# Performance work log

Measured on AMD Instinct MI355X. Metric: run time of the kernel, lower is better.

The kernel has to match this reference:

```python
import jax, jax.numpy as jnp
import numpy as np

B, T, C, H = 8, 2048, 384, 64

def setup_inputs() -> dict:
    key = jax.random.key(0)
    k1, k2, k3, k4 = jax.random.split(key, 4)
    x = jax.random.normal(k1, (B, T, C), dtype=jnp.float32)
    Wq = jax.random.normal(k2, (C, H), dtype=jnp.float32) * (C ** -0.5)
    Wk = jax.random.normal(k3, (C, H), dtype=jnp.float32) * (C ** -0.5)
    Wv = jax.random.normal(k4, (C, H), dtype=jnp.float32) * (C ** -0.5)
    return {"x": x, "Wq": Wq, "Wk": Wk, "Wv": Wv}

def reference(x, Wq, Wk, Wv):
    # x: (B, T, C); projections: (B, T, H)
    Bn, Tn, Cn = x.shape
    q = jnp.einsum('btc,ch->bth', x, Wq)
    k = jnp.einsum('btc,ch->bth', x, Wk)
    v = jnp.einsum('btc,ch->bth', x, Wv)
    # NOTE: source scales by C**-0.5 (embedding dim), not head_size**-0.5
    weights = jnp.einsum('bth,bsh->bts', q, k) * (Cn ** -0.5)  # (B, T, T)
    causal = jnp.tril(jnp.ones((Tn, Tn), dtype=bool))
    weights = jnp.where(causal, weights, -jnp.inf)
    # NOTE: source applies softmax over dim=1 (query/row axis), reproduced faithfully
    weights = jax.nn.softmax(weights, axis=1)
    # dropout omitted (eval-mode reference)
    return jnp.einsum('bts,bsh->bth', weights, v)
```

## Files before the change

### kernel.cpp

```cpp
#include <hip/hip_runtime.h>
#include <hip/hip_bf16.h>
#include <math.h>

#define Bn 8
#define Tn 2048
#define Cn 384
#define Hn 64
#define SCALE2 0.07362241f

using bf16x8 = __attribute__((ext_vector_type(8))) short;
using f32x4  = __attribute__((ext_vector_type(4))) float;
using u32x4  = __attribute__((ext_vector_type(4))) unsigned;

#define MFMA(a, b, c) __builtin_amdgcn_mfma_f32_16x16x32_bf16((a), (b), (c), 0, 0, 0)

static __device__ __forceinline__ short f2bf(float f) {
  unsigned u = __float_as_uint(f);
  u += 0x7fffu + ((u >> 16) & 1u);
  return (short)(u >> 16);
}
static __device__ __forceinline__ float bf2f(short s) {
  return __uint_as_float(((unsigned)(unsigned short)s) << 16);
}
static __device__ __forceinline__ float fexp2(float x) {
#if __has_builtin(__builtin_amdgcn_exp2f)
  return __builtin_amdgcn_exp2f(x);
#else
  return exp2f(x);
#endif
}
static __device__ __forceinline__ unsigned pack2(float lo, float hi) {
  return (unsigned)(unsigned short)f2bf(lo) | ((unsigned)(unsigned short)f2bf(hi) << 16);
}

__global__ __launch_bounds__(256) void wconv_kernel(
    const float* __restrict__ Wq, const float* __restrict__ Wk,
    const float* __restrict__ Wv, short* __restrict__ WbT) {
  int idx = blockIdx.x * 256 + threadIdx.x;
  int n = idx / 384, k = idx - n * 384;
  const float* W = (n < 64) ? Wq : (n < 128) ? Wk : Wv;
  WbT[idx] = f2bf(W[k * 64 + (n & 63)]);
}

__global__ __launch_bounds__(256) void proj_kernel(
    const float* __restrict__ x, const short* __restrict__ WbT,
    short* __restrict__ qb, short* __restrict__ kb, short* __restrict__ vT) {
  __shared__ short xs[16][392];
  __shared__ short vtile[64][20];
  const int tid = threadIdx.x;
  const int t0 = blockIdx.x * 16;
  const float* xb = x + (size_t)t0 * Cn;
  #pragma unroll
  for (int i = 0; i < 6; ++i) {
    int j = tid + i * 256;
    int row = j / 96, colv = (j - row * 96) * 4;
    float4 v = *(const float4*)(xb + row * Cn + colv);
    short4 s4; s4.x = f2bf(v.x); s4.y = f2bf(v.y); s4.z = f2bf(v.z); s4.w = f2bf(v.w);
    *(short4*)(&xs[row][colv]) = s4;
  }
  __syncthreads();
  const int w = tid >> 6, l15 = tid & 15, quad = (tid & 63) >> 4;
  f32x4 acc[3] = {};
  for (int ks = 0; ks < 12; ++ks) {
    bf16x8 a = *(const bf16x8*)(&xs[l15][ks * 32 + quad * 8]);
    #pragma unroll
    for (int cf = 0; cf < 3; ++cf) {
      bf16x8 bfr = *(const bf16x8*)(WbT + (size_t)(48 * w + 16 * cf + l15) * Cn + ks * 32 + quad * 8);
      acc[cf] = MFMA(a, bfr, acc[cf]);
    }
  }
  #pragma unroll
  for (int cf = 0; cf < 3; ++cf) {
    int cbase = 48 * w + 16 * cf, c = cbase + l15;
    #pragma unroll
    for (int r = 0; r < 4; ++r) {
      int row = t0 + quad * 4 + r;
      short val = f2bf(acc[cf][r]);
      if (cbase < 64)       qb[(size_t)row * Hn + c] = val;
      else if (cbase < 128) kb[(size_t)row * Hn + (c - 64)] = val;
      else                  vtile[c - 128][quad * 4 + r] = val;
    }
  }
  __syncthreads();
  const int b = t0 >> 11, t0l = t0 & 2047;
  int h = tid >> 2, tseg = (tid & 3) * 4;
  *(short4*)(vT + ((size_t)(b * Hn + h)) * Tn + t0l + tseg) =
      *(const short4*)(&vtile[h][tseg]);
}

__global__ __launch_bounds__(256) void colstats_kernel(
    const short* __restrict__ qb, const short* __restrict__ kb,
    float* __restrict__ pL) {
  const int unit = blockIdx.x;
  const int b = unit >> 7, rem = unit & 127;
  const int j = rem >> 3, u = rem & 7;
  const int lo = (u * 33) >> 3, hi = ((u + 1) * 33) >> 3;
  const int big = 32 - j;
  const int tid = threadIdx.x, w = tid >> 6, l15 = tid & 15, quad = (tid & 63) >> 4;
  __shared__ float redl[64][17];

  auto run = [&](const int i, const int k0, const int k1, const int slot) {
    const int s0 = i << 6;
    float l[4] = {0.f, 0.f, 0.f, 0.f};
    const int n = k1 - k0;
    if (n > 0) {
      bf16x8 bk[8];
      #pragma unroll
      for (int nf = 0; nf < 4; ++nf) {
        const size_t krow = (size_t)(b * Tn + s0 + 16 * nf + l15) * Hn;
        bk[2 * nf]     = *(const bf16x8*)(kb + krow + quad * 8);
        bk[2 * nf + 1] = *(const bf16x8*)(kb + krow + 32 + quad * 8);
      }
      auto cload = [&](bf16x8& A0, bf16x8& A1, int k) {
        size_t ar = (size_t)(b * Tn + ((i + k) << 6) + 16 * w + l15) * Hn;
        A0 = *(const bf16x8*)(qb + ar + quad * 8);
        A1 = *(const bf16x8*)(qb + ar + 32 + quad * 8);
      };
      auto ccomp = [&](bf16x8 A0, bf16x8 A1, int k) {
        f32x4 sc[4] = {};
        #pragma unroll
        for (int nf = 0; nf < 4; ++nf) {
          sc[nf] = MFMA(A0, bk[2 * nf], sc[nf]);
          sc[nf] = MFMA(A1, bk[2 * nf + 1], sc[nf]);
        }
        const bool diag = (k == 0);
        const int tb = ((i + k) << 6) + 16 * w + quad * 4;
        #pragma unroll
        for (int nf = 0; nf < 4; ++nf) {
          int s = s0 + 16 * nf + l15;
          #pragma unroll
          for (int r = 0; r < 4; ++r) {
            float v = sc[nf][r] * SCALE2;
            if (diag && (tb + r) < s) v = -INFINITY;
            l[nf] += fexp2(v);
          }
        }
      };
      bf16x8 a0A, a1A, a0B, a1B, a0C, a1C;
      cload(a0A, a1A, k0);
      if (n > 1) cload(a0B, a1B, k0 + 1);
      if (n > 2) cload(a0C, a1C, k0 + 2);
      int k = k0;
      while (k + 3 < k1) {
        ccomp(a0A, a1A, k);     cload(a0A, a1A, k + 3);
        ccomp(a0B, a1B, k + 1); if (k + 4 < k1) cload(a0B, a1B, k + 4);
        ccomp(a0C, a1C, k + 2); if (k + 5 < k1) cload(a0C, a1C, k + 5);
        k += 3;
      }
      const int rem2 = k1 - k;
      if (rem2 > 0) ccomp(a0A, a1A, k);
      if (rem2 > 1) ccomp(a0B, a1B, k + 1);
      if (rem2 > 2) ccomp(a0C, a1C, k + 2);
    }
    __syncthreads();
    #pragma unroll
    for (int nf = 0; nf < 4; ++nf) redl[16 * nf + l15][w * 4 + quad] = l[nf];
    __syncthreads();
    if (tid < 64) {
      float ls = 0.f;
      #pragma unroll
      for (int q2 = 0; q2 < 16; ++q2) ls += redl[tid][q2];
      pL[unit * 128 + slot * 64 + tid] = ls;
    }
  };
  run(j, lo, min(hi, big), 0);
  run(31 - j, max(lo, big) - big, hi - big, 1);
}

__global__ __launch_bounds__(256) void vhat_kernel(
    const short* __restrict__ vT, const float* __restrict__ pL,
    short* __restrict__ vS, float* __restrict__ outz) {
  int gid = blockIdx.x * 256 + threadIdx.x;
  size_t base = (size_t)gid * 8;
  int b = (int)(base >> 17), s = (int)(base & 2047);
  int i = s >> 6, c = s & 63;
  int j2 = (i < 16) ? i : 31 - i;
  int slot = (i < 16) ? 0 : 1;
  const float* pp = pL + (size_t)((b * 16 + j2) * 8) * 128 + slot * 64 + c;
  float L0x = 0.f, L0y = 0.f, L0z = 0.f, L0w = 0.f;
  float L1x = 0.f, L1y = 0.f, L1z = 0.f, L1w = 0.f;
  #pragma unroll
  for (int u = 0; u < 8; ++u) {
    float4 p0 = *(const float4*)(pp + u * 128);
    float4 p1 = *(const float4*)(pp + u * 128 + 4);
    L0x += p0.x; L0y += p0.y; L0z += p0.z; L0w += p0.w;
    L1x += p1.x; L1y += p1.y; L1z += p1.z; L1w += p1.w;
  }
  short4 v0 = *(const short4*)(vT + base);
  short4 v1 = *(const short4*)(vT + base + 4);
  short4 r0, r1;
  r0.x = f2bf(bf2f(v0.x) / L0x); r0.y = f2bf(bf2f(v0.y) / L0y);
  r0.z = f2bf(bf2f(v0.z) / L0z); r0.w = f2bf(bf2f(v0.w) / L0w);
  r1.x = f2bf(bf2f(v1.x) / L1x); r1.y = f2bf(bf2f(v1.y) / L1y);
  r1.z = f2bf(bf2f(v1.z) / L1z); r1.w = f2bf(bf2f(v1.w) / L1w);
  *(short4*)(vS + base) = r0;
  *(short4*)(vS + base + 4) = r1;
  float4 z = {0.f, 0.f, 0.f, 0.f};
  *(float4*)(outz + base) = z;
  *(float4*)(outz + base + 4) = z;
}

__global__ __launch_bounds__(256) void outg_kernel(
    const short* __restrict__ qb, const short* __restrict__ kb,
    const short* __restrict__ vS, float* __restrict__ out) {
  const int unit = blockIdx.x;
  const int b = unit >> 7, rem = unit & 127;
  const int j = rem >> 3, u = rem & 7;
  const int lo = (u * 33) >> 3, hi = ((u + 1) * 33) >> 3;
  const int big = 32 - j;
  const int tid = threadIdx.x, w = tid >> 6, l15 = tid & 15, quad = (tid & 63) >> 4;
  __shared__ unsigned plds_raw[4][512];
  char* pw = (char*)(&plds_raw[w][0]);
  const int swz = (l15 & 7) << 4;
  int wroff[8];
  #pragma unroll
  for (int nf = 0; nf < 4; ++nf)
    #pragma unroll
    for (int p = 0; p < 2; ++p)
      wroff[2 * nf + p] = l15 * 128 + ((nf * 32 + quad * 8 + p * 4) ^ swz);
  const int rd0 = l15 * 128 + ((quad * 16) ^ swz);
  const int rd1 = l15 * 128 + ((64 + quad * 16) ^ swz);
  const size_t QKbase = (size_t)b * Tn * Hn;
  const size_t Vbase  = (size_t)b * Hn * Tn;

  auto run = [&](const int tile, const int k0, const int k1) {
    if (k0 >= k1) return;
    const int tbase = (tile << 6) + 16 * w;
    const size_t qrow = QKbase + (size_t)(tbase + l15) * Hn;
    const bf16x8 qf0 = *(const bf16x8*)(qb + qrow + quad * 8);
    const bf16x8 qf1 = *(const bf16x8*)(qb + qrow + 32 + quad * 8);
    const int tg = tbase + l15;
    f32x4 acc[4] = {};
    bf16x8 kf[8];
    auto loadK = [&](int ch) {
      const int s0 = ch << 6;
      #pragma unroll
      for (int nf = 0; nf < 4; ++nf) {
        const size_t kr = QKbase + (size_t)(s0 + 16 * nf + l15) * Hn;
        kf[2 * nf]     = *(const bf16x8*)(kb + kr + quad * 8);
        kf[2 * nf + 1] = *(const bf16x8*)(kb + kr + 32 + quad * 8);
      }
    };
    loadK(k0);
    for (int ch = k0; ch < k1; ++ch) {
      const int s0 = ch << 6;
      f32x4 sc[4] = {};
      #pragma unroll
      for (int nf = 0; nf < 4; ++nf) {
        sc[nf] = MFMA(kf[2 * nf], qf0, sc[nf]);
        sc[nf] = MFMA(kf[2 * nf + 1], qf1, sc[nf]);
      }
      if (ch + 1 < k1) loadK(ch + 1);
      bf16x8 vf[8];
      #pragma unroll
      for (int nf = 0; nf < 4; ++nf) {
        const size_t vr = Vbase + (size_t)(16 * nf + l15) * Tn + s0;
        vf[2 * nf]     = *(const bf16x8*)(vS + vr + quad * 8);
        vf[2 * nf + 1] = *(const bf16x8*)(vS + vr + 32 + quad * 8);
      }
      const bool diag = (ch == tile);
      #pragma unroll
      for (int nf = 0; nf < 4; ++nf) {
        float ev[4];
        #pragma unroll
        for (int r = 0; r < 4; ++r) {
          float v = sc[nf][r] * SCALE2;
          const int s = s0 + 16 * nf + quad * 4 + r;
          if (diag && tg < s) v = -INFINITY;
          ev[r] = fexp2(v);
        }
        *(unsigned*)(pw + wroff[2 * nf])     = pack2(ev[0], ev[1]);
        *(unsigned*)(pw + wroff[2 * nf + 1]) = pack2(ev[2], ev[3]);
      }
      __asm__ __volatile__("" ::: "memory");
      const bf16x8 a0 = __builtin_bit_cast(bf16x8, *(const u32x4*)(pw + rd0));
      const bf16x8 a1 = __builtin_bit_cast(bf16x8, *(const u32x4*)(pw + rd1));
      #pragma unroll
      for (int nf = 0; nf < 4; ++nf) {
        acc[nf] = MFMA(a0, vf[2 * nf], acc[nf]);
        acc[nf] = MFMA(a1, vf[2 * nf + 1], acc[nf]);
      }
    }
    #pragma unroll
    for (int nf = 0; nf < 4; ++nf)
      #pragma unroll
      for (int r = 0; r < 4; ++r)
        atomicAdd(&out[QKbase + (size_t)(tbase + quad * 4 + r) * Hn + 16 * nf + l15],
                  acc[nf][r]);
  };
  run(31 - j, lo, min(hi, big));
  run(j, max(lo, big) - big, hi - big);
}

extern "C" void kernel_launch(void* const* d_in, const int* in_sizes, int n_in,
                              void* d_out, int out_size, void* d_ws, size_t ws_size,
                              hipStream_t stream) {
  const float* x  = (const float*)d_in[0];
  const float* Wq = (const float*)d_in[1];
  const float* Wk = (const float*)d_in[2];
  const float* Wv = (const float*)d_in[3];
  char* ws = (char*)d_ws;
  short* qb   = (short*)(ws);
  short* kb   = (short*)(ws + 2097152);
  short* vT   = (short*)(ws + 4194304);
  short* vS   = (short*)(ws + 6291456);
  short* WbT  = (short*)(ws + 8388608);
  float* pL   = (float*)(ws + 8536064);
  float* outp = (float*)d_out;

  hipLaunchKernelGGL(wconv_kernel, dim3(288), dim3(256), 0, stream, Wq, Wk, Wv, WbT);
  hipLaunchKernelGGL(proj_kernel, dim3(Bn * Tn / 16), dim3(256), 0, stream, x, WbT, qb, kb, vT);
  hipLaunchKernelGGL(colstats_kernel, dim3(1024), dim3(256), 0, stream, qb, kb, pL);
  hipLaunchKernelGGL(vhat_kernel, dim3(512), dim3(256), 0, stream, vT, pL, vS, outp);
  hipLaunchKernelGGL(outg_kernel, dim3(1024), dim3(256), 0, stream, qb, kb, vS, outp);
}
```

Measured before the change: 162.5 us.

## Split key chunks across waves per 16-row strip and reduce in LDS, dropping atomics

Reworks the output kernel so each block handles one 16-row query strip of a tile, with its four waves striding over key chunks. Partial accumulators are reduced through shared memory and written with plain stores, replacing global atomicAdds and the zero-fill of the output in vhat_kernel. It also prefetches V one chunk ahead, orders blocks so the largest tiles launch first, and sets a launch-bounds occupancy hint. The cost is duplicated Q/K reads per strip, a new LDS reduction buffer, and wave imbalance on small tiles.

```diff
diff --git a/kernel.cpp b/kernel.cpp
--- a/kernel.cpp
+++ b/kernel.cpp
@@ -169,7 +169,7 @@
 
 __global__ __launch_bounds__(256) void vhat_kernel(
     const short* __restrict__ vT, const float* __restrict__ pL,
-    short* __restrict__ vS, float* __restrict__ outz) {
+    short* __restrict__ vS) {
   int gid = blockIdx.x * 256 + threadIdx.x;
   size_t base = (size_t)gid * 8;
   int b = (int)(base >> 17), s = (int)(base & 2047);
@@ -195,101 +195,113 @@
   r1.z = f2bf(bf2f(v1.z) / L1z); r1.w = f2bf(bf2f(v1.w) / L1w);
   *(short4*)(vS + base) = r0;
   *(short4*)(vS + base + 4) = r1;
-  float4 z = {0.f, 0.f, 0.f, 0.f};
-  *(float4*)(outz + base) = z;
-  *(float4*)(outz + base + 4) = z;
-}
-
-__global__ __launch_bounds__(256) void outg_kernel(
+}
+
+__global__ __launch_bounds__(256, 3) void outg_kernel(
     const short* __restrict__ qb, const short* __restrict__ kb,
     const short* __restrict__ vS, float* __restrict__ out) {
-  const int unit = blockIdx.x;
-  const int b = unit >> 7, rem = unit & 127;
-  const int j = rem >> 3, u = rem & 7;
-  const int lo = (u * 33) >> 3, hi = ((u + 1) * 33) >> 3;
-  const int big = 32 - j;
+  const int bid = blockIdx.x;
+  const int tile = 31 - (bid >> 5);
+  const int sub = bid & 31;
+  const int b = sub >> 2, strip = sub & 3;
+  const int nch = tile + 1;
   const int tid = threadIdx.x, w = tid >> 6, l15 = tid & 15, quad = (tid & 63) >> 4;
-  __shared__ unsigned plds_raw[4][512];
-  char* pw = (char*)(&plds_raw[w][0]);
+  __shared__ unsigned plds[4][512];
+  __shared__ float red[4][16][64];
   const int swz = (l15 & 7) << 4;
   int wroff[8];
   #pragma unroll
   for (int nf = 0; nf < 4; ++nf)
     #pragma unroll
     for (int p = 0; p < 2; ++p)
-      wroff[2 * nf + p] = l15 * 128 + ((nf * 32 + quad * 8 + p * 4) ^ swz);
-  const int rd0 = l15 * 128 + ((quad * 16) ^ swz);
-  const int rd1 = l15 * 128 + ((64 + quad * 16) ^ swz);
+      wroff[2 * nf + p] = (l15 * 128 + ((nf * 32 + quad * 8 + p * 4) ^ swz)) >> 2;
+  const int rd0 = (l15 * 128 + ((quad * 16) ^ swz)) >> 2;
+  const int rd1 = (l15 * 128 + ((64 + quad * 16) ^ swz)) >> 2;
   const size_t QKbase = (size_t)b * Tn * Hn;
   const size_t Vbase  = (size_t)b * Hn * Tn;
-
-  auto run = [&](const int tile, const int k0, const int k1) {
-    if (k0 >= k1) return;
-    const int tbase = (tile << 6) + 16 * w;
-    const size_t qrow = QKbase + (size_t)(tbase + l15) * Hn;
-    const bf16x8 qf0 = *(const bf16x8*)(qb + qrow + quad * 8);
-    const bf16x8 qf1 = *(const bf16x8*)(qb + qrow + 32 + quad * 8);
-    const int tg = tbase + l15;
-    f32x4 acc[4] = {};
-    bf16x8 kf[8];
-    auto loadK = [&](int ch) {
-      const int s0 = ch << 6;
+  const int tbase = (tile << 6) + 16 * strip;
+  const int tg = tbase + l15;
+
+  const size_t qrow = QKbase + (size_t)(tbase + l15) * Hn;
+  const bf16x8 qf0 = *(const bf16x8*)(qb + qrow + quad * 8);
+  const bf16x8 qf1 = *(const bf16x8*)(qb + qrow + 32 + quad * 8);
+
+  f32x4 acc[4] = {};
+  bf16x8 kf[8], vf[8];
+  auto loadK = [&](int ch) {
+    const int s0 = ch << 6;
+    #pragma unroll
+    for (int nf = 0; nf < 4; ++nf) {
+      const size_t kr = QKbase + (size_t)(s0 + 16 * nf + l15) * Hn;
+      kf[2 * nf]     = *(const bf16x8*)(kb + kr + quad * 8);
+      kf[2 * nf + 1] = *(const bf16x8*)(kb + kr + 32 + quad * 8);
+    }
+  };
+  auto loadV = [&](int ch) {
+    const int s0 = ch << 6;
+    #pragma unroll
+    for (int nf = 0; nf < 4; ++nf) {
+      const size_t vr = Vbase + (size_t)(16 * nf + l15) * Tn + s0;
+      vf[2 * nf]     = *(const bf16x8*)(vS + vr + quad * 8);
+      vf[2 * nf + 1] = *(const bf16x8*)(vS + vr + 32 + quad * 8);
+    }
+  };
+
+  if (w < nch) { loadK(w); loadV(w); }
+  for (int ch = w; ch < nch; ch += 4) {
+    const int s0 = ch << 6;
+    f32x4 sc[4] = {};
+    #pragma unroll
+    for (int nf = 0; nf < 4; ++nf) {
+      sc[nf] = MFMA(kf[2 * nf], qf0, sc[nf]);
+      sc[nf] = MFMA(kf[2 * nf + 1], qf1, sc[nf]);
+    }
+    const int nx = ch + 4;
+    if (nx < nch) loadK(nx);
+    const bool diag = (ch == tile);
+    #pragma unroll
+    for (int nf = 0; nf < 4; ++nf) {
+      float ev[4];
       #pragma unroll
-      for (int nf = 0; nf < 4; ++nf) {
-        const size_t kr = QKbase + (size_t)(s0 + 16 * nf + l15) * Hn;
-        kf[2 * nf]     = *(const bf16x8*)(kb + kr + quad * 8);
-        kf[2 * nf + 1] = *(const bf16x8*)(kb + kr + 32 + quad * 8);
+      for (int r = 0; r < 4; ++r) {
+        float v = sc[nf][r] * SCALE2;
+        const int s = s0 + 16 * nf + quad * 4 + r;
+        if (diag && tg < s) v = -INFINITY;
+        ev[r] = fexp2(v);
       }
-    };
-    loadK(k0);
-    for (int ch = k0; ch < k1; ++ch) {
-      const int s0 = ch << 6;
-      f32x4 sc[4] = {};
-      #pragma unroll
-      for (int nf = 0; nf < 4; ++nf) {
-        sc[nf] = MFMA(kf[2 * nf], qf0, sc[nf]);
-        sc[nf] = MFMA(kf[2 * nf + 1], qf1, sc[nf]);
-      }
-      if (ch + 1 < k1) loadK(ch + 1);
-      bf16x8 vf[8];
-      #pragma unroll
-      for (int nf = 0; nf < 4; ++nf) {
-        const size_t vr = Vbase + (size_t)(16 * nf + l15) * Tn + s0;
-        vf[2 * nf]     = *(const bf16x8*)(vS + vr + quad * 8);
-        vf[2 * nf + 1] = *(const bf16x8*)(vS + vr + 32 + quad * 8);
-      }
-      const bool diag = (ch == tile);
-      #pragma unroll
-      for (int nf = 0; nf < 4; ++nf) {
-        float ev[4];
-        #pragma unroll
-        for (int r = 0; r < 4; ++r) {
-          float v = sc[nf][r] * SCALE2;
-          const int s = s0 + 16 * nf + quad * 4 + r;
-          if (diag && tg < s) v = -INFINITY;
-          ev[r] = fexp2(v);
-        }
-        *(unsigned*)(pw + wroff[2 * nf])     = pack2(ev[0], ev[1]);
-        *(unsigned*)(pw + wroff[2 * nf + 1]) = pack2(ev[2], ev[3]);
-      }
-      __asm__ __volatile__("" ::: "memory");
-      const bf16x8 a0 = __builtin_bit_cast(bf16x8, *(const u32x4*)(pw + rd0));
-      const bf16x8 a1 = __builtin_bit_cast(bf16x8, *(const u32x4*)(pw + rd1));
-      #pragma unroll
-      for (int nf = 0; nf < 4; ++nf) {
-        acc[nf] = MFMA(a0, vf[2 * nf], acc[nf]);
-        acc[nf] = MFMA(a1, vf[2 * nf + 1], acc[nf]);
-      }
-    }
-    #pragma unroll
-    for (int nf = 0; nf < 4; ++nf)
-      #pragma unroll
-      for (int r = 0; r < 4; ++r)
-        atomicAdd(&out[QKbase + (size_t)(tbase + quad * 4 + r) * Hn + 16 * nf + l15],
-                  acc[nf][r]);
-  };
-  run(31 - j, lo, min(hi, big));
-  run(j, max(lo, big) - big, hi - big);
+      plds[w][wroff[2 * nf]]     = pack2(ev[0], ev[1]);
+      plds[w][wroff[2 * nf + 1]] = pack2(ev[2], ev[3]);
+    }
+    __asm__ __volatile__("" ::: "memory");
+    const bf16x8 a0 = __builtin_bit_cast(bf16x8, *(const u32x4*)(&plds[w][rd0]));
+    const bf16x8 a1 = __builtin_bit_cast(bf16x8, *(const u32x4*)(&plds[w][rd1]));
+    #pragma unroll
+    for (int nf = 0; nf < 4; ++nf) {
+      acc[nf] = MFMA(a0, vf[2 * nf], acc[nf]);
+      acc[nf] = MFMA(a1, vf[2 * nf + 1], acc[nf]);
+    }
+    if (nx < nch) loadV(nx);
+  }
+
+  #pragma unroll
+  for (int nf = 0; nf < 4; ++nf)
+    #pragma unroll
+    for (int r = 0; r < 4; ++r)
+      red[w][quad * 4 + r][16 * nf + l15] = acc[nf][r];
+  __syncthreads();
+  {
+    const int row = tid >> 4, c4 = (tid & 15) * 4;
+    float4 s0 = *(const float4*)(&red[0][row][c4]);
+    float4 s1 = *(const float4*)(&red[1][row][c4]);
+    float4 s2 = *(const float4*)(&red[2][row][c4]);
+    float4 s3 = *(const float4*)(&red[3][row][c4]);
+    float4 t;
+    t.x = (s0.x + s1.x) + (s2.x + s3.x);
+    t.y = (s0.y + s1.y) + (s2.y + s3.y);
+    t.z = (s0.z + s1.z) + (s2.z + s3.z);
+    t.w = (s0.w + s1.w) + (s2.w + s3.w);
+    *(float4*)(&out[QKbase + (size_t)(tbase + row) * Hn + c4]) = t;
+  }
 }
 
 extern "C" void kernel_launch(void* const* d_in, const int* in_sizes, int n_in,
@@ -311,6 +323,6 @@
   hipLaunchKernelGGL(wconv_kernel, dim3(288), dim3(256), 0, stream, Wq, Wk, Wv, WbT);
   hipLaunchKernelGGL(proj_kernel, dim3(Bn * Tn / 16), dim3(256), 0, stream, x, WbT, qb, kb, vT);
   hipLaunchKernelGGL(colstats_kernel, dim3(1024), dim3(256), 0, stream, qb, kb, pL);
-  hipLaunchKernelGGL(vhat_kernel, dim3(512), dim3(256), 0, stream, vT, pL, vS, outp);
+  hipLaunchKernelGGL(vhat_kernel, dim3(512), dim3(256), 0, stream, vT, pL, vS);
   hipLaunchKernelGGL(outg_kernel, dim3(1024), dim3(256), 0, stream, qb, kb, vS, outp);
 }
```

After: 147.5 us. -9.2%, faster.
